# Optimization experiments

Hardware: AMD Instinct MI355X
Metric: run time of the kernel (lower is better)

Reference implementation:

```python
import jax, jax.numpy as jnp
import numpy as np
import math

B, S, H, NH = 4, 2048, 768, 12
HD = H // NH
EPS = 1e-12

def setup_inputs() -> dict:
    key = jax.random.key(0)
    ks = jax.random.split(key, 12)
    sc = 0.02
    return {
        "hidden_states": jax.random.normal(ks[0], (B, S, H), jnp.float32),
        "attention_mask": jnp.zeros((B, 1, 1, S), jnp.float32),
        "Wq": jax.random.normal(ks[1], (H, H), jnp.float32) * sc,
        "bq": jnp.zeros((H,), jnp.float32),
        "Wk": jax.random.normal(ks[2], (H, H), jnp.float32) * sc,
        "bk": jnp.zeros((H,), jnp.float32),
        "Wv": jax.random.normal(ks[3], (H, H), jnp.float32) * sc,
        "bv": jnp.zeros((H,), jnp.float32),
        "Wo": jax.random.normal(ks[4], (H, H), jnp.float32) * sc,
        "bo": jnp.zeros((H,), jnp.float32),
        "ln_g": jnp.ones((H,), jnp.float32),
        "ln_b": jnp.zeros((H,), jnp.float32),
    }

def _heads(x):
    # [B,S,H] -> [B,NH,S,HD]
    return x.reshape(B, S, NH, HD).transpose(0, 2, 1, 3)

def reference(hidden_states, attention_mask, Wq, bq, Wk, bk, Wv, bv, Wo, bo, ln_g, ln_b):
    q = _heads(hidden_states @ Wq.T + bq)
    k = _heads(hidden_states @ Wk.T + bk)
    v = _heads(hidden_states @ Wv.T + bv)
    # eager attention: [B,NH,S,S]
    scores = jnp.einsum("bhqd,bhkd->bhqk", q, k) / math.sqrt(HD)
    scores = scores + attention_mask
    probs = jax.nn.softmax(scores, axis=-1)
    ctx = jnp.einsum("bhqk,bhkd->bhqd", probs, v)
    ctx = ctx.transpose(0, 2, 1, 3).reshape(B, S, H)
    # output dense + residual + LayerNorm (dropout is identity in eval)
    h = ctx @ Wo.T + bo + hidden_states
    mu = jnp.mean(h, axis=-1, keepdims=True)
    var = jnp.mean(jnp.square(h - mu), axis=-1, keepdims=True)
    out = (h - mu) * jax.lax.rsqrt(var + EPS) * ln_g + ln_b
    return out
```

## Files before the change

### kernel.cpp

```cpp
#include <hip/hip_runtime.h>
#include <math.h>

#define B_  4
#define S_  2048
#define H_  768
#define NH_ 12
#define HD_ 64
#define M_  (B_*S_)
#define K_  768

using bf16x8 = __attribute__((ext_vector_type(8))) short;
using s16x4  = __attribute__((ext_vector_type(4))) short;
using f32x4  = __attribute__((ext_vector_type(4))) float;

__device__ inline short f2bf(float f) {
    union { float f; unsigned u; } v{f};
    unsigned r = (v.u + 0x7FFF + ((v.u >> 16) & 1)) >> 16;
    return (short)r;
}

#define GLDS16(g, l) __builtin_amdgcn_global_load_lds( \
    (const __attribute__((address_space(1))) void*)(g), \
    (__attribute__((address_space(3))) void*)(l), 16, 0, 0)

__device__ inline const bf16x8* LDSRD(const short* base, int row, int colByte) {
    return (const bf16x8*)((const char*)base + ((row << 7) + (colByte ^ ((row & 7) << 4))));
}

__global__ __launch_bounds__(256)
void cvt5(const float* __restrict__ s0, const float* __restrict__ s1,
          const float* __restrict__ s2, const float* __restrict__ s3,
          const float* __restrict__ s4,
          short* __restrict__ d0, short* __restrict__ d1,
          short* __restrict__ d2, short* __restrict__ d3,
          short* __restrict__ d4) {
    const int r = blockIdx.y;
    const float* s = r == 0 ? s0 : r == 1 ? s1 : r == 2 ? s2 : r == 3 ? s3 : s4;
    short* d      = r == 0 ? d0 : r == 1 ? d1 : r == 2 ? d2 : r == 3 ? d3 : d4;
    const int n4  = (r == 0 ? M_ * H_ : H_ * H_) >> 2;
    for (int i = blockIdx.x * blockDim.x + threadIdx.x; i < n4; i += gridDim.x * blockDim.x) {
        float4 v = ((const float4*)s)[i];
        s16x4 o;
        o[0] = f2bf(v.x); o[1] = f2bf(v.y); o[2] = f2bf(v.z); o[3] = f2bf(v.w);
        ((s16x4*)d)[i] = o;
    }
}

template<int MODE>
__global__ __launch_bounds__(256)
void gemm_bf16(const short* __restrict__ A, const short* __restrict__ Bw,
               const float* __restrict__ bias, const float* __restrict__ res,
               void* __restrict__ out, float scale) {
    __shared__ __align__(16) short As[128 * 32];
    __shared__ __align__(16) short Bs[128 * 32];
    const int tid = threadIdx.x;
    const int w = tid >> 6, l = tid & 63;
    const int l16 = l & 15, lg = l >> 4;
    const int wm = w >> 1, wn = w & 1;
    const int m0 = blockIdx.x * 128, n0 = blockIdx.y * 128;

    f32x4 acc[4][4];
    #pragma unroll
    for (int mi = 0; mi < 4; mi++)
        #pragma unroll
        for (int ni = 0; ni < 4; ni++)
            acc[mi][ni][0] = acc[mi][ni][1] = acc[mi][ni][2] = acc[mi][ni][3] = 0.f;

    for (int k0 = 0; k0 < K_; k0 += 32) {
        #pragma unroll
        for (int i = 0; i < 2; i++) {
            const int o = w * 2048 + i * 1024 + l * 16;
            const int row = o >> 6, colb = o & 63;
            const char* ga = (const char*)A  + (((size_t)(m0 + row)) * K_ + k0) * 2 + colb;
            const char* gb = (const char*)Bw + (((size_t)(n0 + row)) * K_ + k0) * 2 + colb;
            GLDS16(ga, (char*)As + w * 2048 + i * 1024);
            GLDS16(gb, (char*)Bs + w * 2048 + i * 1024);
        }
        __syncthreads();

        bf16x8 af[4], bfr[4];
        #pragma unroll
        for (int mi = 0; mi < 4; mi++)
            af[mi] = *(const bf16x8*)&As[(wm * 64 + mi * 16 + l16) * 32 + lg * 8];
        #pragma unroll
        for (int ni = 0; ni < 4; ni++)
            bfr[ni] = *(const bf16x8*)&Bs[(wn * 64 + ni * 16 + l16) * 32 + lg * 8];
        #pragma unroll
        for (int mi = 0; mi < 4; mi++)
            #pragma unroll
            for (int ni = 0; ni < 4; ni++)
                acc[mi][ni] = __builtin_amdgcn_mfma_f32_16x16x32_bf16(af[mi], bfr[ni], acc[mi][ni], 0, 0, 0);
        __syncthreads();
    }

    float bcol[4];
    #pragma unroll
    for (int ni = 0; ni < 4; ni++) bcol[ni] = bias[n0 + wn * 64 + ni * 16 + l16];

    if (MODE == 0) {
        short* obf = (short*)out;
        const int h = blockIdx.y * 2 + wn;
        #pragma unroll
        for (int mi = 0; mi < 4; mi++) {
            #pragma unroll
            for (int r = 0; r < 4; r++) {
                const int row = m0 + wm * 64 + mi * 16 + lg * 4 + r;
                const int bb = row >> 11, ss = row & 2047;
                const size_t base = (((size_t)(bb * NH_ + h)) * S_ + ss) * HD_;
                #pragma unroll
                for (int ni = 0; ni < 4; ni++)
                    obf[base + ni * 16 + l16] = f2bf((acc[mi][ni][r] + bcol[ni]) * scale);
            }
        }
    } else {
        float* o = (float*)out;
        #pragma unroll
        for (int mi = 0; mi < 4; mi++) {
            #pragma unroll
            for (int r = 0; r < 4; r++) {
                const int row = m0 + wm * 64 + mi * 16 + lg * 4 + r;
                #pragma unroll
                for (int ni = 0; ni < 4; ni++) {
                    const int col = n0 + wn * 64 + ni * 16 + l16;
                    o[(size_t)row * H_ + col] = acc[mi][ni][r] + bcol[ni] + res[(size_t)row * H_ + col];
                }
            }
        }
    }
}

__global__ __launch_bounds__(256)
void transpose_v(const short* __restrict__ vin, short* __restrict__ vout) {
    __shared__ __align__(16) short L[4096];
    const int bh = blockIdx.y, st = blockIdx.x * 64;
    const int t = threadIdx.x;
    const int sl = t >> 2, d0 = (t & 3) * 16;
    const short* g = vin + ((size_t)bh * S_ + st + sl) * HD_ + d0;
    #pragma unroll
    for (int u = 0; u < 2; u++) {
        const int cb = (d0 + u * 8) * 2;
        *(bf16x8*)((char*)L + (sl << 7) + (cb ^ ((sl & 7) << 4))) = *(const bf16x8*)(g + u * 8);
    }
    __syncthreads();
    const int d = t >> 2, s0 = (t & 3) * 16;
    short tmp[16];
    #pragma unroll
    for (int j = 0; j < 16; j++) {
        const int row = s0 + j;
        tmp[j] = *(const short*)((const char*)L + (row << 7) + ((d * 2) ^ ((row & 7) << 4)));
    }
    short* o = vout + ((size_t)bh * HD_ + d) * S_ + st + s0;
    *(bf16x8*)(o)     = *(bf16x8*)&tmp[0];
    *(bf16x8*)(o + 8) = *(bf16x8*)&tmp[8];
}

__global__ __launch_bounds__(256)
void flash_attn_mfma(const short* __restrict__ q, const short* __restrict__ k,
                     const short* __restrict__ vt, const float* __restrict__ mask,
                     short* __restrict__ ctx) {
    const int qt = blockIdx.x, h = blockIdx.y, b = blockIdx.z;
    __shared__ __align__(16) short KsL[4096];
    __shared__ __align__(16) short VtL[4096];
    __shared__ __align__(16) short PsL[4096];
    const int tid = threadIdx.x;
    const int w = tid >> 6, l = tid & 63;
    const int l16 = l & 15, lg = l >> 4;

    const size_t qrow = ((size_t)(b * NH_ + h)) * S_ + qt * 64 + w * 16 + l16;
    bf16x8 qf0 = *(const bf16x8*)(q + qrow * HD_ + lg * 8);
    bf16x8 qf1 = *(const bf16x8*)(q + qrow * HD_ + 32 + lg * 8);

    const size_t kbase  = ((size_t)(b * NH_ + h)) * S_ * HD_;
    const size_t vtbase = ((size_t)(b * NH_ + h)) * HD_ * S_;

    f32x4 oacc[4];
    #pragma unroll
    for (int i = 0; i < 4; i++) oacc[i][0] = oacc[i][1] = oacc[i][2] = oacc[i][3] = 0.f;
    float m_reg = -3.0e38f, l_reg = 0.f;

    for (int ct = 0; ct < S_ / 64; ct++) {
        #pragma unroll
        for (int i = 0; i < 2; i++) {
            const int o = (w * 2 + i) * 1024 + l * 16;
            const int row = o >> 7;
            const int cb = (o & 127) ^ ((row & 7) << 4);
            const char* gk = (const char*)(k  + kbase  + (size_t)(ct * 64 + row) * HD_) + cb;
            const char* gv = (const char*)(vt + vtbase + (size_t)row * S_ + ct * 64) + cb;
            GLDS16(gk, (char*)KsL + o);
            GLDS16(gv, (char*)VtL + o);
        }
        __syncthreads();

        f32x4 sacc[4];
        #pragma unroll
        for (int n = 0; n < 4; n++) {
            sacc[n][0] = sacc[n][1] = sacc[n][2] = sacc[n][3] = 0.f;
            bf16x8 kb0 = *LDSRD(KsL, n * 16 + l16, lg * 16);
            bf16x8 kb1 = *LDSRD(KsL, n * 16 + l16, 64 + lg * 16);
            sacc[n] = __builtin_amdgcn_mfma_f32_16x16x32_bf16(kb0, qf0, sacc[n], 0, 0, 0);
            sacc[n] = __builtin_amdgcn_mfma_f32_16x16x32_bf16(kb1, qf1, sacc[n], 0, 0, 0);
        }

        #pragma unroll
        for (int n = 0; n < 4; n++) {
            float4 mk = *(const float4*)(mask + (size_t)b * S_ + ct * 64 + n * 16 + lg * 4);
            sacc[n][0] += mk.x; sacc[n][1] += mk.y; sacc[n][2] += mk.z; sacc[n][3] += mk.w;
        }

        float pmax = sacc[0][0];
        #pragma unroll
        for (int n = 0; n < 4; n++)
            #pragma unroll
            for (int r = 0; r < 4; r++) pmax = fmaxf(pmax, sacc[n][r]);
        pmax = fmaxf(pmax, __shfl_xor(pmax, 16));
        pmax = fmaxf(pmax, __shfl_xor(pmax, 32));
        const float mn = fmaxf(m_reg, pmax);
        const float corr = __expf(m_reg - mn);
        float rs = 0.f;
        #pragma unroll
        for (int n = 0; n < 4; n++)
            #pragma unroll
            for (int r = 0; r < 4; r++) {
                sacc[n][r] = __expf(sacc[n][r] - mn);
                rs += sacc[n][r];
            }
        rs += __shfl_xor(rs, 16);
        rs += __shfl_xor(rs, 32);
        l_reg = l_reg * corr + rs;
        m_reg = mn;

        const int prow = w * 16 + l16;
        #pragma unroll
        for (int n = 0; n < 4; n++) {
            s16x4 pk;
            pk[0] = f2bf(sacc[n][0]); pk[1] = f2bf(sacc[n][1]);
            pk[2] = f2bf(sacc[n][2]); pk[3] = f2bf(sacc[n][3]);
            *(s16x4*)((char*)PsL + (prow << 7) + ((32 * n + 8 * lg) ^ ((prow & 7) << 4))) = pk;
        }

        float corr4[4];
        #pragma unroll
        for (int r = 0; r < 4; r++) corr4[r] = __shfl(corr, lg * 4 + r);
        #pragma unroll
        for (int nd = 0; nd < 4; nd++)
            #pragma unroll
            for (int r = 0; r < 4; r++) oacc[nd][r] *= corr4[r];

        bf16x8 pa0 = *LDSRD(PsL, prow, lg * 16);
        bf16x8 pa1 = *LDSRD(PsL, prow, 64 + lg * 16);
        #pragma unroll
        for (int nd = 0; nd < 4; nd++) {
            bf16x8 vb0 = *LDSRD(VtL, nd * 16 + l16, lg * 16);
            bf16x8 vb1 = *LDSRD(VtL, nd * 16 + l16, 64 + lg * 16);
            oacc[nd] = __builtin_amdgcn_mfma_f32_16x16x32_bf16(pa0, vb0, oacc[nd], 0, 0, 0);
            oacc[nd] = __builtin_amdgcn_mfma_f32_16x16x32_bf16(pa1, vb1, oacc[nd], 0, 0, 0);
        }
        __syncthreads();
    }

    #pragma unroll
    for (int r = 0; r < 4; r++) {
        const float inv = 1.f / __shfl(l_reg, lg * 4 + r);
        const size_t row = (size_t)(b * S_ + qt * 64 + w * 16 + lg * 4 + r);
        #pragma unroll
        for (int nd = 0; nd < 4; nd++)
            ctx[row * H_ + h * HD_ + nd * 16 + l16] = f2bf(oacc[nd][r] * inv);
    }
}

__global__ __launch_bounds__(256)
void layernorm_k(const float* __restrict__ hin, const float* __restrict__ g,
                 const float* __restrict__ beta, float* __restrict__ out) {
    const int row = blockIdx.x;
    const int tid = threadIdx.x;
    const float* x = hin + (size_t)row * H_;
    __shared__ float sm[4];

    float v0 = x[tid], v1 = x[tid + 256], v2 = x[tid + 512];
    float s = v0 + v1 + v2;
    #pragma unroll
    for (int o = 32; o > 0; o >>= 1) s += __shfl_xor(s, o);
    if ((tid & 63) == 0) sm[tid >> 6] = s;
    __syncthreads();
    float mu = (sm[0] + sm[1] + sm[2] + sm[3]) * (1.f / 768.f);

    float d0 = v0 - mu, d1 = v1 - mu, d2 = v2 - mu;
    float ss = d0*d0 + d1*d1 + d2*d2;
    #pragma unroll
    for (int o = 32; o > 0; o >>= 1) ss += __shfl_xor(ss, o);
    __syncthreads();
    if ((tid & 63) == 0) sm[tid >> 6] = ss;
    __syncthreads();
    float var = (sm[0] + sm[1] + sm[2] + sm[3]) * (1.f / 768.f);
    float sc = rsqrtf(var + 1e-12f);

    float* y = out + (size_t)row * H_;
    y[tid]       = d0 * sc * g[tid]       + beta[tid];
    y[tid + 256] = d1 * sc * g[tid + 256] + beta[tid + 256];
    y[tid + 512] = d2 * sc * g[tid + 512] + beta[tid + 512];
}

extern "C" void kernel_launch(void* const* d_in, const int* in_sizes, int n_in,
                              void* d_out, int out_size, void* d_ws, size_t ws_size,
                              hipStream_t stream) {
    const float* hs   = (const float*)d_in[0];
    const float* mask = (const float*)d_in[1];
    const float* Wq   = (const float*)d_in[2];
    const float* bq   = (const float*)d_in[3];
    const float* Wk   = (const float*)d_in[4];
    const float* bk   = (const float*)d_in[5];
    const float* Wv   = (const float*)d_in[6];
    const float* bv   = (const float*)d_in[7];
    const float* Wo   = (const float*)d_in[8];
    const float* bo   = (const float*)d_in[9];
    const float* ln_g = (const float*)d_in[10];
    const float* ln_b = (const float*)d_in[11];
    float* out = (float*)d_out;

    const size_t MH = (size_t)M_ * H_;
    const size_t HH = (size_t)H_ * H_;
    short* hsbf = (short*)d_ws;
    short* wqbf = hsbf + MH;
    short* wkbf = wqbf + HH;
    short* wvbf = wkbf + HH;
    short* wobf = wvbf + HH;
    short* qbf  = wobf + HH;
    short* kbf  = qbf + MH;
    short* vbf  = kbf + MH;
    short* vtb  = vbf + MH;
    short* cbf  = vtb + MH;
    float* hb   = (float*)(cbf + MH);

    cvt5<<<dim3(256, 5), 256, 0, stream>>>(hs, Wq, Wk, Wv, Wo,
                                           hsbf, wqbf, wkbf, wvbf, wobf);

    dim3 gg(M_ / 128, H_ / 128);
    gemm_bf16<0><<<gg, 256, 0, stream>>>(hsbf, wqbf, bq, nullptr, qbf, 0.125f);
    gemm_bf16<0><<<gg, 256, 0, stream>>>(hsbf, wkbf, bk, nullptr, kbf, 1.0f);
    gemm_bf16<0><<<gg, 256, 0, stream>>>(hsbf, wvbf, bv, nullptr, vbf, 1.0f);

    transpose_v<<<dim3(S_ / 64, B_ * NH_), 256, 0, stream>>>(vbf, vtb);

    flash_attn_mfma<<<dim3(S_ / 64, NH_, B_), 256, 0, stream>>>(qbf, kbf, vtb, mask, cbf);

    gemm_bf16<1><<<gg, 256, 0, stream>>>(cbf, wobf, bo, hs, hb, 1.0f);

    layernorm_k<<<M_, 256, 0, stream>>>(hb, ln_g, ln_b, out);
}
```

Measured before the change: 225.8 us.

## Use exp2 softmax with folded log2e, lazy rescaling, and packed bf16 convert

Folds log2(e) into the Q projection scale and into a pre-scaled copy of the mask, so the attention softmax can use the hardware exp2 instead of expf. It also skips the running-max update and the output-accumulator rescale unless some row's max grows by more than 8 (in log2 units), and replaces the manual bf16 rounding with the packed v_cvt_pk_bf16_f32 instruction. The aim is fewer VALU ops in the attention inner loop. The cost is an extra small kernel launch and extra workspace, plus slightly looser numerics because probabilities may reach up to 2^8 before being rescaled.

```diff
diff --git a/kernel.cpp b/kernel.cpp
--- a/kernel.cpp
+++ b/kernel.cpp
@@ -8,6 +8,7 @@
 #define HD_ 64
 #define M_  (B_*S_)
 #define K_  768
+#define LOG2E 1.44269504088896340736f
 
 using bf16x8 = __attribute__((ext_vector_type(8))) short;
 using s16x4  = __attribute__((ext_vector_type(4))) short;
@@ -17,6 +18,12 @@
     union { float f; unsigned u; } v{f};
     unsigned r = (v.u + 0x7FFF + ((v.u >> 16) & 1)) >> 16;
     return (short)r;
+}
+
+__device__ inline unsigned cvt_pk_bf16(float lo, float hi) {
+    unsigned r;
+    asm("v_cvt_pk_bf16_f32 %0, %1, %2" : "=v"(r) : "v"(lo), "v"(hi));
+    return r;
 }
 
 #define GLDS16(g, l) __builtin_amdgcn_global_load_lds( \
@@ -46,6 +53,12 @@
     }
 }
 
+__global__ __launch_bounds__(256)
+void scale_mask(const float* __restrict__ m, float* __restrict__ o) {
+    const int i = blockIdx.x * 256 + threadIdx.x;
+    if (i < B_ * S_) o[i] = m[i] * LOG2E;
+}
+
 template<int MODE>
 __global__ __launch_bounds__(256)
 void gemm_bf16(const short* __restrict__ A, const short* __restrict__ Bw,
@@ -207,44 +220,48 @@
             sacc[n][0] += mk.x; sacc[n][1] += mk.y; sacc[n][2] += mk.z; sacc[n][3] += mk.w;
         }
 
-        float pmax = sacc[0][0];
-        #pragma unroll
-        for (int n = 0; n < 4; n++)
-            #pragma unroll
-            for (int r = 0; r < 4; r++) pmax = fmaxf(pmax, sacc[n][r]);
+        float x0 = fmaxf(fmaxf(sacc[0][0], sacc[0][1]), fmaxf(sacc[0][2], sacc[0][3]));
+        float x1 = fmaxf(fmaxf(sacc[1][0], sacc[1][1]), fmaxf(sacc[1][2], sacc[1][3]));
+        float x2 = fmaxf(fmaxf(sacc[2][0], sacc[2][1]), fmaxf(sacc[2][2], sacc[2][3]));
+        float x3 = fmaxf(fmaxf(sacc[3][0], sacc[3][1]), fmaxf(sacc[3][2], sacc[3][3]));
+        float pmax = fmaxf(fmaxf(x0, x1), fmaxf(x2, x3));
         pmax = fmaxf(pmax, __shfl_xor(pmax, 16));
         pmax = fmaxf(pmax, __shfl_xor(pmax, 32));
-        const float mn = fmaxf(m_reg, pmax);
-        const float corr = __expf(m_reg - mn);
+
+        if (!__all(pmax - m_reg <= 8.f)) {
+            const float mn = fmaxf(m_reg, pmax);
+            const float corr = __builtin_amdgcn_exp2f(m_reg - mn);
+            l_reg *= corr;
+            m_reg = mn;
+            float corr4[4];
+            #pragma unroll
+            for (int r = 0; r < 4; r++) corr4[r] = __shfl(corr, lg * 4 + r);
+            #pragma unroll
+            for (int nd = 0; nd < 4; nd++)
+                #pragma unroll
+                for (int r = 0; r < 4; r++) oacc[nd][r] *= corr4[r];
+        }
+
         float rs = 0.f;
         #pragma unroll
         for (int n = 0; n < 4; n++)
             #pragma unroll
             for (int r = 0; r < 4; r++) {
-                sacc[n][r] = __expf(sacc[n][r] - mn);
+                sacc[n][r] = __builtin_amdgcn_exp2f(sacc[n][r] - m_reg);
                 rs += sacc[n][r];
             }
         rs += __shfl_xor(rs, 16);
         rs += __shfl_xor(rs, 32);
-        l_reg = l_reg * corr + rs;
-        m_reg = mn;
+        l_reg += rs;
 
         const int prow = w * 16 + l16;
         #pragma unroll
         for (int n = 0; n < 4; n++) {
-            s16x4 pk;
-            pk[0] = f2bf(sacc[n][0]); pk[1] = f2bf(sacc[n][1]);
-            pk[2] = f2bf(sacc[n][2]); pk[3] = f2bf(sacc[n][3]);
-            *(s16x4*)((char*)PsL + (prow << 7) + ((32 * n + 8 * lg) ^ ((prow & 7) << 4))) = pk;
-        }
-
-        float corr4[4];
-        #pragma unroll
-        for (int r = 0; r < 4; r++) corr4[r] = __shfl(corr, lg * 4 + r);
-        #pragma unroll
-        for (int nd = 0; nd < 4; nd++)
-            #pragma unroll
-            for (int r = 0; r < 4; r++) oacc[nd][r] *= corr4[r];
+            uint2 pk;
+            pk.x = cvt_pk_bf16(sacc[n][0], sacc[n][1]);
+            pk.y = cvt_pk_bf16(sacc[n][2], sacc[n][3]);
+            *(uint2*)((char*)PsL + (prow << 7) + ((32 * n + 8 * lg) ^ ((prow & 7) << 4))) = pk;
+        }
 
         bf16x8 pa0 = *LDSRD(PsL, prow, lg * 16);
         bf16x8 pa1 = *LDSRD(PsL, prow, 64 + lg * 16);
@@ -330,18 +347,20 @@
     short* vtb  = vbf + MH;
     short* cbf  = vtb + MH;
     float* hb   = (float*)(cbf + MH);
+    float* msk2 = hb + MH;
 
     cvt5<<<dim3(256, 5), 256, 0, stream>>>(hs, Wq, Wk, Wv, Wo,
                                            hsbf, wqbf, wkbf, wvbf, wobf);
+    scale_mask<<<(B_ * S_ + 255) / 256, 256, 0, stream>>>(mask, msk2);
 
     dim3 gg(M_ / 128, H_ / 128);
-    gemm_bf16<0><<<gg, 256, 0, stream>>>(hsbf, wqbf, bq, nullptr, qbf, 0.125f);
+    gemm_bf16<0><<<gg, 256, 0, stream>>>(hsbf, wqbf, bq, nullptr, qbf, 0.125f * LOG2E);
     gemm_bf16<0><<<gg, 256, 0, stream>>>(hsbf, wkbf, bk, nullptr, kbf, 1.0f);
     gemm_bf16<0><<<gg, 256, 0, stream>>>(hsbf, wvbf, bv, nullptr, vbf, 1.0f);
 
     transpose_v<<<dim3(S_ / 64, B_ * NH_), 256, 0, stream>>>(vbf, vtb);
 
-    flash_attn_mfma<<<dim3(S_ / 64, NH_, B_), 256, 0, stream>>>(qbf, kbf, vtb, mask, cbf);
+    flash_attn_mfma<<<dim3(S_ / 64, NH_, B_), 256, 0, stream>>>(qbf, kbf, vtb, msk2, cbf);
 
     gemm_bf16<1><<<gg, 256, 0, stream>>>(cbf, wobf, bo, hs, hb, 1.0f);
 
```

After: 237.6 us. 5.2% more time.
